# Kernel tuning notes

Hardware: AMD Instinct MI355X
Metric: run time of the kernel (lower is better)

Reference implementation:

```python
import jax, jax.numpy as jnp
import numpy as np

D = 1024; NH = 16; HD = 64; FF = 4096; DEPTH = 4
P = 14; C = 3; GRID = 32; MERGE = 2; NIMG = 4
L = GRID * GRID; S = NIMG * L; ORIG = 24; EPS = 1e-6
SCALE = HD ** -0.5


def setup_inputs() -> dict:
    key = jax.random.key(0)
    ks = jax.random.split(key, 12)
    s = 0.02
    return {
        "pixel_values": jax.random.normal(ks[0], (S, C * P * P), jnp.float32),
        "grid_thw": jnp.tile(jnp.array([[1, GRID, GRID]], jnp.int32), (NIMG, 1)),
        "conv_w": jax.random.normal(ks[1], (D, C * P * P), jnp.float32) * s,
        "conv_b": jnp.zeros((D,), jnp.float32),
        "pos_embed": jax.random.normal(ks[2], (ORIG * ORIG, D), jnp.float32) * s,
        "ln1_g": jnp.ones((DEPTH, D), jnp.float32),
        "ln1_b": jnp.zeros((DEPTH, D), jnp.float32),
        "qkv_w": jax.random.normal(ks[3], (DEPTH, 3 * D, D), jnp.float32) * s,
        "qkv_b": jnp.zeros((DEPTH, 3 * D), jnp.float32),
        "proj_w": jax.random.normal(ks[4], (DEPTH, D, D), jnp.float32) * s,
        "proj_b": jnp.zeros((DEPTH, D), jnp.float32),
        "ln2_g": jnp.ones((DEPTH, D), jnp.float32),
        "ln2_b": jnp.zeros((DEPTH, D), jnp.float32),
        "fc1_w": jax.random.normal(ks[5], (DEPTH, FF, D), jnp.float32) * s,
        "fc1_b": jnp.zeros((DEPTH, FF), jnp.float32),
        "fc2_w": jax.random.normal(ks[6], (DEPTH, D, FF), jnp.float32) * s,
        "fc2_b": jnp.zeros((DEPTH, D), jnp.float32),
    }


def _pos_ids():
    # rot_pos_emb spatial-merge permutation for one t=1 image, tiled over images
    h = jnp.broadcast_to(jnp.arange(GRID)[:, None], (GRID, GRID))
    w = jnp.broadcast_to(jnp.arange(GRID)[None, :], (GRID, GRID))
    def perm(a):
        a = a.reshape(GRID // MERGE, MERGE, GRID // MERGE, MERGE)
        return a.transpose(0, 2, 1, 3).reshape(-1)
    hpos = jnp.tile(perm(h), NIMG)  # [S]
    wpos = jnp.tile(perm(w), NIMG)
    return hpos, wpos


def _bilinear_border(img, nx, ny):
    # img [H, W, D]; nx, ny in [-1, 1]; align_corners=False, padding_mode='border'
    Hh, Ww, _ = img.shape
    x = (nx + 1.0) * 0.5 * Ww - 0.5
    y = (ny + 1.0) * 0.5 * Hh - 0.5
    x0 = jnp.floor(x); y0 = jnp.floor(y)
    wx = (x - x0)[:, None]; wy = (y - y0)[:, None]
    x0i = jnp.clip(x0.astype(jnp.int32), 0, Ww - 1)
    x1i = jnp.clip(x0.astype(jnp.int32) + 1, 0, Ww - 1)
    y0i = jnp.clip(y0.astype(jnp.int32), 0, Hh - 1)
    y1i = jnp.clip(y0.astype(jnp.int32) + 1, 0, Hh - 1)
    v00 = img[y0i, x0i]; v01 = img[y0i, x1i]
    v10 = img[y1i, x0i]; v11 = img[y1i, x1i]
    return (v00 * (1 - wy) * (1 - wx) + v01 * (1 - wy) * wx
            + v10 * wy * (1 - wx) + v11 * wy * wx)


def _ln(x, g, b):
    m = jnp.mean(x, axis=-1, keepdims=True)
    v = jnp.mean(jnp.square(x - m), axis=-1, keepdims=True)
    return (x - m) * jax.lax.rsqrt(v + EPS) * g + b


def _forward(pixel_values, conv_w, conv_b, pos_embed, ln1_g, ln1_b, qkv_w, qkv_b,
             proj_w, proj_b, ln2_g, ln2_b, fc1_w, fc1_b, fc2_w, fc2_b):
    # patch embed: conv with kernel==stride==patch over one patch == linear
    x = pixel_values @ conv_w.T + conv_b  # [S, D]

    # interpolated 2D position embedding (grid_sample bilinear, border pad)
    hpos, wpos = _pos_ids()
    norm_w = (wpos.astype(jnp.float32) + 0.5) / GRID * 2.0 - 1.0
    norm_h = (hpos.astype(jnp.float32) + 0.5) / GRID * 2.0 - 1.0
    pe = _bilinear_border(pos_embed.reshape(ORIG, ORIG, D), norm_w, norm_h)
    x = x + pe

    for i in range(DEPTH):
        # attention (block-diagonal over equal-length images -> batched)
        r = x
        y = _ln(x, ln1_g[i], ln1_b[i])
        qkv = (y @ qkv_w[i].T + qkv_b[i]).reshape(NIMG, L, 3, NH, HD)
        q = qkv[:, :, 0].transpose(0, 2, 1, 3)  # [B, H, L, hd]
        k = qkv[:, :, 1].transpose(0, 2, 1, 3)
        v = qkv[:, :, 2].transpose(0, 2, 1, 3)
        scores = jnp.einsum('bhqd,bhkd->bhqk', q, k) * SCALE
        probs = jax.nn.softmax(scores, axis=-1)
        o = jnp.einsum('bhqk,bhkd->bhqd', probs, v)
        o = o.transpose(0, 2, 1, 3).reshape(S, D)
        x = r + o @ proj_w[i].T + proj_b[i]
        # MLP
        r = x
        y = _ln(x, ln2_g[i], ln2_b[i])
        h = jax.nn.gelu(y @ fc1_w[i].T + fc1_b[i], approximate=False)
        x = r + h @ fc2_w[i].T + fc2_b[i]
    return x


def reference(pixel_values, grid_thw, conv_w, conv_b, pos_embed, ln1_g, ln1_b,
              qkv_w, qkv_b, proj_w, proj_b, ln2_g, ln2_b, fc1_w, fc1_b, fc2_w, fc2_b):
    return _forward(pixel_values, conv_w, conv_b, pos_embed, ln1_g, ln1_b, qkv_w,
                    qkv_b, proj_w, proj_b, ln2_g, ln2_b, fc1_w, fc1_b, fc2_w, fc2_b)
```

## Files before the change

### kernel.cpp

```cpp
#include <hip/hip_runtime.h>
#include <math.h>

typedef __bf16 bf16x8 __attribute__((ext_vector_type(8)));
typedef float f32x4 __attribute__((ext_vector_type(4)));
typedef short s16x4 __attribute__((ext_vector_type(4)));
typedef short s16x8 __attribute__((ext_vector_type(8)));

static __device__ __forceinline__ short f2bs(float f) {
  return __builtin_bit_cast(short, (__bf16)f);
}

#define GLL16(gp, lp) __builtin_amdgcn_global_load_lds( \
    (const __attribute__((address_space(1))) void*)(gp), \
    (__attribute__((address_space(3))) void*)(lp), 16, 0, 0)

__global__ __launch_bounds__(256) void cvt_f32_bf16(const float* __restrict__ s,
                                                    short* __restrict__ d, int n) {
  int stride = gridDim.x * blockDim.x * 4;
  for (int j = (blockIdx.x * blockDim.x + threadIdx.x) * 4; j < n; j += stride) {
    float4 v = *(const float4*)(s + j);
    s16x4 o;
    o[0] = f2bs(v.x); o[1] = f2bs(v.y); o[2] = f2bs(v.z); o[3] = f2bs(v.w);
    *(s16x4*)(d + j) = o;
  }
}

__global__ __launch_bounds__(256) void cvt_pad(const float* __restrict__ s,
                                               short* __restrict__ d) {
  int r = blockIdx.x;
  for (int c = threadIdx.x; c < 608; c += blockDim.x)
    d[(size_t)r * 608 + c] = (c < 588) ? f2bs(s[(size_t)r * 588 + c]) : (short)0;
}

template <int N, int K, int EPI, int CM, int CN>
__global__ __launch_bounds__(256) void gemm_bt(const short* __restrict__ A,
                                               const short* __restrict__ B,
                                               const float* __restrict__ bias,
                                               const float* __restrict__ resid,
                                               void* __restrict__ out) {
  static_assert(K % 32 == 0, "K");
  constexpr int NT = K / 32;
  static_assert(NT >= 3, "pipeline depth");
  constexpr int NX = N / 128, NY = 32;
  constexpr int nwg = NX * NY;
  static_assert(nwg % 8 == 0 && (nwg / 8) % (CM * CN) == 0, "chunk");
  static_assert(NX % CN == 0 && NY % CM == 0, "cells");
  __shared__ short lA[3][128 * 32];
  __shared__ short lB[3][128 * 32];

  const int o = blockIdx.x;
  const int wid = (o & 7) * (nwg / 8) + (o >> 3);
  constexpr int cellsz = CM * CN;
  const int cell = wid / cellsz, within = wid % cellsz;
  constexpr int cellsx = NX / CN;
  const int bm0 = ((cell / cellsx) * CM + within / CN) * 128;
  const int bn0 = ((cell % cellsx) * CN + within % CN) * 128;

  const int t = threadIdx.x, w = t >> 6, lane = t & 63;
  const int wr = w >> 1, wc = w & 1;
  f32x4 acc[4][4] = {};

  const int srow = t >> 2;
  const int scol = ((t & 3) ^ ((srow >> 1) & 3)) * 8;
  const short* aP = A + (size_t)(bm0 + srow) * K + scol;
  const short* bP = B + (size_t)(bn0 + srow) * K + scol;
  const int sdst0 = (w * 16) * 32;
  const int sdst1 = (64 + w * 16) * 32;

  const int lr = lane & 15;
  const int qx = ((lane >> 4) ^ ((lr >> 1) & 3)) * 8;

  auto stage = [&](int buf, int ko) {
    GLL16(aP + ko, &lA[buf][sdst0]);
    GLL16(aP + ko + (size_t)64 * K, &lA[buf][sdst1]);
    GLL16(bP + ko, &lB[buf][sdst0]);
    GLL16(bP + ko + (size_t)64 * K, &lB[buf][sdst1]);
  };

  stage(0, 0);
  stage(1, 32);
  stage(2, 64);

  int buf = 0;
  for (int kt = 0; kt < NT; ++kt) {
    if (kt < NT - 2)       asm volatile("s_waitcnt vmcnt(8)" ::: "memory");
    else if (kt == NT - 2) asm volatile("s_waitcnt vmcnt(4)" ::: "memory");
    else                   asm volatile("s_waitcnt vmcnt(0)" ::: "memory");
    __builtin_amdgcn_s_barrier();
    asm volatile("" ::: "memory");
    __builtin_amdgcn_sched_barrier(0);

    bf16x8 af[4], bg[4];
#pragma unroll
    for (int mi = 0; mi < 4; ++mi)
      af[mi] = *(const bf16x8*)&lA[buf][(wr * 64 + mi * 16 + lr) * 32 + qx];
#pragma unroll
    for (int ni = 0; ni < 4; ++ni)
      bg[ni] = *(const bf16x8*)&lB[buf][(wc * 64 + ni * 16 + lr) * 32 + qx];

    asm volatile("s_waitcnt lgkmcnt(0)" ::: "memory");
    __builtin_amdgcn_sched_barrier(0);
    __builtin_amdgcn_s_barrier();
    asm volatile("" ::: "memory");
    __builtin_amdgcn_sched_barrier(0);

    if (kt + 3 < NT) stage(buf, (kt + 3) * 32);
    __builtin_amdgcn_sched_barrier(0);

#pragma unroll
    for (int mi = 0; mi < 4; ++mi)
#pragma unroll
      for (int ni = 0; ni < 4; ++ni)
        acc[mi][ni] = __builtin_amdgcn_mfma_f32_16x16x32_bf16(af[mi], bg[ni],
                                                              acc[mi][ni], 0, 0, 0);
    buf = (buf == 2) ? 0 : buf + 1;
  }

  const int lg4 = (lane >> 4) * 4;
#pragma unroll
  for (int mi = 0; mi < 4; ++mi) {
#pragma unroll
    for (int ni = 0; ni < 4; ++ni) {
      const int row = bm0 + wr * 64 + mi * 16 + lg4;
      const int col = bn0 + wc * 64 + ni * 16 + lr;
      const float bc = bias[col];
#pragma unroll
      for (int r = 0; r < 4; ++r) {
        float v = acc[mi][ni][r] + bc;
        size_t idx = (size_t)(row + r) * N + col;
        if constexpr (EPI == 1) v = 0.5f * v * (1.0f + erff(v * 0.70710678118f));
        if constexpr (EPI == 0 || EPI == 1) ((short*)out)[idx] = f2bs(v);
        else if constexpr (EPI == 2) ((float*)out)[idx] = v + resid[idx];
        else ((float*)out)[idx] = v;
      }
    }
  }
}

__global__ __launch_bounds__(256) void ln_fwd(const float* __restrict__ x,
                                              const float* __restrict__ g,
                                              const float* __restrict__ b,
                                              short* __restrict__ y) {
  const int row = blockIdx.x, t = threadIdx.x, w = t >> 6, lane = t & 63;
  const float4 v = ((const float4*)(x + (size_t)row * 1024))[t];
  float s = v.x + v.y + v.z + v.w;
  float ss = v.x * v.x + v.y * v.y + v.z * v.z + v.w * v.w;
#pragma unroll
  for (int m = 1; m < 64; m <<= 1) { s += __shfl_xor(s, m); ss += __shfl_xor(ss, m); }
  __shared__ float rs[4], rss[4];
  if (lane == 0) { rs[w] = s; rss[w] = ss; }
  __syncthreads();
  s = rs[0] + rs[1] + rs[2] + rs[3];
  ss = rss[0] + rss[1] + rss[2] + rss[3];
  const float mean = s * (1.f / 1024.f);
  const float var = ss * (1.f / 1024.f) - mean * mean;
  const float rstd = rsqrtf(var + 1e-6f);
  const float4 gv = ((const float4*)g)[t];
  const float4 bv = ((const float4*)b)[t];
  s16x4 o;
  o[0] = f2bs((v.x - mean) * rstd * gv.x + bv.x);
  o[1] = f2bs((v.y - mean) * rstd * gv.y + bv.y);
  o[2] = f2bs((v.z - mean) * rstd * gv.z + bv.z);
  o[3] = f2bs((v.w - mean) * rstd * gv.w + bv.w);
  *(s16x4*)(y + (size_t)row * 1024 + t * 4) = o;
}

__global__ __launch_bounds__(256) void pos_add(float* __restrict__ x,
                                               const float* __restrict__ pe) {
  const int sidx = blockIdx.x;
  const int f = sidx & 1023;
  const int wq = 2 * ((f >> 2) & 15) + (f & 1);
  const int hq = 2 * (f >> 6) + ((f >> 1) & 1);
  const float gx = (wq + 0.5f) * 0.75f - 0.5f;
  const float gy = (hq + 0.5f) * 0.75f - 0.5f;
  const float fx = floorf(gx), fy = floorf(gy);
  const float wx = gx - fx, wy = gy - fy;
  int x0 = (int)fx, y0 = (int)fy;
  const int x0i = x0 < 0 ? 0 : (x0 > 23 ? 23 : x0);
  const int x1i = (x0 + 1) < 0 ? 0 : ((x0 + 1) > 23 ? 23 : x0 + 1);
  const int y0i = y0 < 0 ? 0 : (y0 > 23 ? 23 : y0);
  const int y1i = (y0 + 1) < 0 ? 0 : ((y0 + 1) > 23 ? 23 : y0 + 1);
  const float w00 = (1 - wy) * (1 - wx), w01 = (1 - wy) * wx;
  const float w10 = wy * (1 - wx), w11 = wy * wx;
  const int c = threadIdx.x * 4;
  const float4 p00 = *(const float4*)(pe + (size_t)(y0i * 24 + x0i) * 1024 + c);
  const float4 p01 = *(const float4*)(pe + (size_t)(y0i * 24 + x1i) * 1024 + c);
  const float4 p10 = *(const float4*)(pe + (size_t)(y1i * 24 + x0i) * 1024 + c);
  const float4 p11 = *(const float4*)(pe + (size_t)(y1i * 24 + x1i) * 1024 + c);
  float* xp = x + (size_t)sidx * 1024 + c;
  float4 xv = *(float4*)xp;
  xv.x += w00 * p00.x + w01 * p01.x + w10 * p10.x + w11 * p11.x;
  xv.y += w00 * p00.y + w01 * p01.y + w10 * p10.y + w11 * p11.y;
  xv.z += w00 * p00.z + w01 * p01.z + w10 * p10.z + w11 * p11.z;
  xv.w += w00 * p00.w + w01 * p01.w + w10 * p10.w + w11 * p11.w;
  *(float4*)xp = xv;
}

__global__ __launch_bounds__(256) void attn_fwd(const short* __restrict__ qkv,
                                                short* __restrict__ outp) {
  __shared__ short lK[2][64 * 64];
  __shared__ short Vt[2][64 * 72];
  const int t = threadIdx.x, w = t >> 6, lane = t & 63;
  const int b = blockIdx.y >> 4, h = blockIdx.y & 15;
  const int sbase = b * 1024;
  const int q0 = blockIdx.x * 64 + w * 16;
  const int lr = lane & 15, lg = lane >> 4;

  const short* qrow = qkv + (size_t)(sbase + q0 + lr) * 3072 + h * 64;
  const bf16x8 qf0 = *(const bf16x8*)(qrow + lg * 8);
  const bf16x8 qf1 = *(const bf16x8*)(qrow + 32 + lg * 8);

  const int krofs = t >> 3;
  const int kcol = ((t & 7) ^ (krofs & 7)) * 8;
  const short* ksrc = qkv + (size_t)(sbase + krofs) * 3072 + 1024 + h * 64 + kcol;
  const int vkv = t >> 2, vdp = t & 3;
  const short* vsrc = qkv + (size_t)(sbase + vkv) * 3072 + 2048 + h * 64 + vdp * 16;
  const int vph = vkv ^ (vdp << 4);

  f32x4 o[4] = {};
  float mrun = -1e30f, lsum = 0.f;

  s16x8 v0 = *(const s16x8*)vsrc;
  s16x8 v1 = *(const s16x8*)(vsrc + 8);
  GLL16(ksrc, &lK[0][(w * 8) * 64]);
  GLL16(ksrc + (size_t)32 * 3072, &lK[0][(32 + w * 8) * 64]);
#pragma unroll
  for (int j = 0; j < 8; ++j) Vt[0][(vdp * 16 + j) * 72 + vph] = v0[j];
#pragma unroll
  for (int j = 0; j < 8; ++j) Vt[0][(vdp * 16 + 8 + j) * 72 + vph] = v1[j];
  asm volatile("s_waitcnt vmcnt(0) lgkmcnt(0)" ::: "memory");
  __builtin_amdgcn_s_barrier();

  int buf = 0;
  for (int kb = 0; kb < 16; ++kb) {
    if (kb < 15) {
      const short* vs = vsrc + (size_t)(kb + 1) * 64 * 3072;
      v0 = *(const s16x8*)vs;
      v1 = *(const s16x8*)(vs + 8);
      const short* ks = ksrc + (size_t)(kb + 1) * 64 * 3072;
      GLL16(ks, &lK[buf ^ 1][(w * 8) * 64]);
      GLL16(ks + (size_t)32 * 3072, &lK[buf ^ 1][(32 + w * 8) * 64]);
    }

    f32x4 s[4];
    __builtin_amdgcn_s_setprio(1);
#pragma unroll
    for (int sub = 0; sub < 4; ++sub) {
      const int krow = (sub * 16 + lr) * 64;
      const bf16x8 kf0 = *(const bf16x8*)&lK[buf][krow + (lg ^ (lr & 7)) * 8];
      const bf16x8 kf1 = *(const bf16x8*)&lK[buf][krow + ((lg + 4) ^ (lr & 7)) * 8];
      f32x4 a = {};
      a = __builtin_amdgcn_mfma_f32_16x16x32_bf16(kf0, qf0, a, 0, 0, 0);
      a = __builtin_amdgcn_mfma_f32_16x16x32_bf16(kf1, qf1, a, 0, 0, 0);
      s[sub] = a;
    }
    __builtin_amdgcn_s_setprio(0);

    constexpr float SC = 0.125f * 1.44269504089f;
    float sl[16];
#pragma unroll
    for (int sub = 0; sub < 4; ++sub)
#pragma unroll
      for (int r = 0; r < 4; ++r) sl[sub * 4 + r] = s[sub][r] * SC;
    float tm = sl[0];
#pragma unroll
    for (int i = 1; i < 16; ++i) tm = fmaxf(tm, sl[i]);
    tm = fmaxf(tm, __shfl_xor(tm, 16));
    tm = fmaxf(tm, __shfl_xor(tm, 32));
    if (!__all(tm <= mrun + 12.0f)) {
      const float newm = fmaxf(mrun, tm);
      const float sc = exp2f(mrun - newm);
      lsum *= sc;
#pragma unroll
      for (int f = 0; f < 4; ++f) {
        o[f][0] *= sc; o[f][1] *= sc; o[f][2] *= sc; o[f][3] *= sc;
      }
      mrun = newm;
    }
    s16x4 pb[4];
    float psum = 0.f;
#pragma unroll
    for (int sub = 0; sub < 4; ++sub)
#pragma unroll
      for (int r = 0; r < 4; ++r) {
        const float p = exp2f(sl[sub * 4 + r] - mrun);
        psum += p;
        pb[sub][r] = f2bs(p);
      }
    psum += __shfl_xor(psum, 16);
    psum += __shfl_xor(psum, 32);
    lsum += psum;

    __builtin_amdgcn_s_setprio(1);
#pragma unroll
    for (int f = 0; f < 4; ++f) {
      const int vrow = (f * 16 + lr) * 72;
#pragma unroll
      for (int sub = 0; sub < 4; ++sub) {
        const s16x4 va = *(const s16x4*)&Vt[buf][vrow + ((sub ^ f) << 4) + lg * 4];
        o[f] = __builtin_amdgcn_mfma_f32_16x16x16bf16_1k(va, pb[sub], o[f], 0, 0, 0);
      }
    }
    __builtin_amdgcn_s_setprio(0);

    if (kb < 15) {
#pragma unroll
      for (int j = 0; j < 8; ++j) Vt[buf ^ 1][(vdp * 16 + j) * 72 + vph] = v0[j];
#pragma unroll
      for (int j = 0; j < 8; ++j) Vt[buf ^ 1][(vdp * 16 + 8 + j) * 72 + vph] = v1[j];
      asm volatile("s_waitcnt vmcnt(0) lgkmcnt(0)" ::: "memory");
      __builtin_amdgcn_s_barrier();
      buf ^= 1;
    }
  }

  const float inv = 1.0f / lsum;
  short* orow = outp + (size_t)(sbase + q0 + lr) * 1024 + h * 64;
#pragma unroll
  for (int f = 0; f < 4; ++f) {
    s16x4 ov;
    ov[0] = f2bs(o[f][0] * inv); ov[1] = f2bs(o[f][1] * inv);
    ov[2] = f2bs(o[f][2] * inv); ov[3] = f2bs(o[f][3] * inv);
    *(s16x4*)(orow + f * 16 + lg * 4) = ov;
  }
}

extern "C" void kernel_launch(void* const* d_in, const int* in_sizes, int n_in,
                              void* d_out, int out_size, void* d_ws, size_t ws_size,
                              hipStream_t stream) {
  const float* pixel  = (const float*)d_in[0];
  const float* conv_w = (const float*)d_in[2];
  const float* conv_b = (const float*)d_in[3];
  const float* pos_e  = (const float*)d_in[4];
  const float* ln1_g  = (const float*)d_in[5];
  const float* ln1_b  = (const float*)d_in[6];
  const float* qkv_w  = (const float*)d_in[7];
  const float* qkv_b  = (const float*)d_in[8];
  const float* proj_w = (const float*)d_in[9];
  const float* proj_b = (const float*)d_in[10];
  const float* ln2_g  = (const float*)d_in[11];
  const float* ln2_b  = (const float*)d_in[12];
  const float* fc1_w  = (const float*)d_in[13];
  const float* fc1_b  = (const float*)d_in[14];
  const float* fc2_w  = (const float*)d_in[15];
  const float* fc2_b  = (const float*)d_in[16];

  char* ws = (char*)d_ws;
  short* wQKV  = (short*)(ws + 0);
  short* wPROJ = (short*)(ws + 25165824);
  short* wFC1  = (short*)(ws + 33554432);
  short* wFC2  = (short*)(ws + 67108864);
  float* X     = (float*)(ws + 100663296);
  short* Y     = (short*)(ws + 117440512);
  short* QKVB  = (short*)(ws + 125829120);
  short* ATTNO = (short*)(ws + 150994944);
  short* H     = QKVB;
  short* WPIX  = QKVB;
  short* WCONV = (short*)(ws + 125829120 + 4980736);

  cvt_f32_bf16<<<2048, 256, 0, stream>>>(qkv_w, wQKV, 4 * 3072 * 1024);
  cvt_f32_bf16<<<1024, 256, 0, stream>>>(proj_w, wPROJ, 4 * 1024 * 1024);
  cvt_f32_bf16<<<2048, 256, 0, stream>>>(fc1_w, wFC1, 4 * 4096 * 1024);
  cvt_f32_bf16<<<2048, 256, 0, stream>>>(fc2_w, wFC2, 4 * 1024 * 4096);
  cvt_pad<<<4096, 256, 0, stream>>>(pixel, WPIX);
  cvt_pad<<<1024, 256, 0, stream>>>(conv_w, WCONV);

  gemm_bt<1024, 608, 3, 4, 8><<<256, 256, 0, stream>>>(WPIX, WCONV, conv_b, nullptr, X);
  pos_add<<<4096, 256, 0, stream>>>(X, pos_e);

  for (int i = 0; i < 4; ++i) {
    ln_fwd<<<4096, 256, 0, stream>>>(X, ln1_g + i * 1024, ln1_b + i * 1024, Y);
    gemm_bt<3072, 1024, 0, 8, 12><<<768, 256, 0, stream>>>(
        Y, wQKV + (size_t)i * 3072 * 1024, qkv_b + i * 3072, nullptr, QKVB);
    attn_fwd<<<dim3(16, 64), 256, 0, stream>>>(QKVB, ATTNO);
    gemm_bt<1024, 1024, 2, 4, 8><<<256, 256, 0, stream>>>(
        ATTNO, wPROJ + (size_t)i * 1024 * 1024, proj_b + i * 1024, X, X);
    ln_fwd<<<4096, 256, 0, stream>>>(X, ln2_g + i * 1024, ln2_b + i * 1024, Y);
    gemm_bt<4096, 1024, 1, 16, 8><<<1024, 256, 0, stream>>>(
        Y, wFC1 + (size_t)i * 4096 * 1024, fc1_b + i * 4096, nullptr, H);
    float* dest = (i < 3) ? X : (float*)d_out;
    gemm_bt<1024, 4096, 2, 4, 8><<<256, 256, 0, stream>>>(
        H, wFC2 + (size_t)i * 1024 * 4096, fc2_b + i * 1024, X, dest);
  }
}
```

Baseline: 1.043 ms.

## Add 256x256-tile 512-thread pipelined GEMM for QKV and FC1 projections

Introduces a new GEMM kernel with 256x256 output tiles, 8 waves per block, double-buffered LDS staged through global_load_lds, a phased schedule that interleaves LDS reads, MFMA bursts and prefetches with explicit barriers and waitcnts, plus an XCD-aware block remap. The QKV and FC1 GEMMs switch to it. The aim is more operand reuse per LDS load and better overlap of memory traffic with MFMA. The cost is fewer blocks (192 and 256) and a higher register and LDS footprint, which can limit occupancy on the machine.

```diff
diff --git a/kernel.cpp b/kernel.cpp
--- a/kernel.cpp
+++ b/kernel.cpp
@@ -132,6 +132,141 @@
         if constexpr (EPI == 0 || EPI == 1) ((short*)out)[idx] = f2bs(v);
         else if constexpr (EPI == 2) ((float*)out)[idx] = v + resid[idx];
         else ((float*)out)[idx] = v;
+      }
+    }
+  }
+}
+
+template <int N, int K, int EPI, int CM, int CN>
+__global__ __launch_bounds__(512, 2) void gemm256(const short* __restrict__ A,
+                                                  const short* __restrict__ B,
+                                                  const float* __restrict__ bias,
+                                                  void* __restrict__ out) {
+  static_assert(K % 64 == 0, "K");
+  constexpr int NKT = K / 64;
+  static_assert(NKT >= 3 && (NKT % 2) == 0, "ktiles");
+  constexpr int NXT = N / 256, MYT = 16;
+  constexpr int nwg = NXT * MYT;
+  static_assert(nwg % 8 == 0 && (nwg / 8) % (CM * CN) == 0, "chunk");
+  static_assert(NXT % CN == 0 && MYT % CM == 0, "cells");
+
+  __shared__ short sA[2][2][8192];
+  __shared__ short sB[2][2][8192];
+
+  const int o = blockIdx.x;
+  const int wid = (o & 7) * (nwg / 8) + (o >> 3);
+  constexpr int cellsz = CM * CN;
+  const int cell = wid / cellsz, within = wid % cellsz;
+  constexpr int cellsx = NXT / CN;
+  const int bm0 = ((cell / cellsx) * CM + within / CN) * 256;
+  const int bn0 = ((cell % cellsx) * CN + within % CN) * 256;
+
+  const int tid = threadIdx.x, wv = tid >> 6, lane = tid & 63;
+  const int wrow = wv >> 2, wcol = wv & 3;
+  const int lr = lane & 15, lg = lane >> 4;
+
+  const int sr0 = tid >> 2;
+  const int sc0 = ((tid & 3) ^ (sr0 & 3)) * 8;
+  const short* aS0 = A + (size_t)(bm0 + sr0) * K + sc0;
+  const short* bS0 = B + (size_t)(bn0 + sr0) * K + sc0;
+  const int ld0 = wv * 512, ld1 = 4096 + wv * 512;
+
+  auto stageA = [&](int d, int h, int kt) {
+    const int off = kt * 64 + h * 32;
+    GLL16(aS0 + off, &sA[d][h][ld0]);
+    GLL16(aS0 + off + (size_t)128 * K, &sA[d][h][ld1]);
+  };
+  auto stageB = [&](int d, int h, int kt) {
+    const int off = kt * 64 + h * 32;
+    GLL16(bS0 + off, &sB[d][h][ld0]);
+    GLL16(bS0 + off + (size_t)128 * K, &sB[d][h][ld1]);
+  };
+
+  const int chR = (lg ^ (lr & 3)) * 8;
+  const int rA0 = wrow * 128 + lr;
+  const int rB0 = wcol * 64 + lr;
+
+  f32x4 acc[8][4] = {};
+
+  stageA(0, 0, 0); stageB(0, 0, 0);
+  stageA(0, 1, 0); stageB(0, 1, 0);
+  stageA(1, 0, 1); stageB(1, 0, 1);
+  asm volatile("s_waitcnt vmcnt(8)" ::: "memory");
+  __builtin_amdgcn_sched_barrier(0);
+  __builtin_amdgcn_s_barrier();
+
+  bf16x8 af[4], bf[4];
+
+#define LDA(mh, ks, d)                                                        \
+  _Pragma("unroll")                                                           \
+  for (int f = 0; f < 4; ++f)                                                 \
+    af[f] = *(const bf16x8*)&sA[d][ks][(rA0 + (mh)*64 + f * 16) * 32 + chR];
+#define LDB(ks, d)                                                            \
+  _Pragma("unroll")                                                           \
+  for (int n = 0; n < 4; ++n)                                                 \
+    bf[n] = *(const bf16x8*)&sB[d][ks][(rB0 + n * 16) * 32 + chR];
+#define MFMA16(mh)                                                            \
+  __builtin_amdgcn_s_setprio(1);                                              \
+  _Pragma("unroll")                                                           \
+  for (int f = 0; f < 4; ++f)                                                 \
+    _Pragma("unroll")                                                         \
+    for (int n = 0; n < 4; ++n)                                               \
+      acc[(mh)*4 + f][n] = __builtin_amdgcn_mfma_f32_16x16x32_bf16(           \
+          af[f], bf[n], acc[(mh)*4 + f][n], 0, 0, 0);                         \
+  __builtin_amdgcn_s_setprio(0);
+#define PH_BAR1                                                               \
+  __builtin_amdgcn_s_barrier();                                               \
+  asm volatile("s_waitcnt lgkmcnt(0)" ::: "memory");                          \
+  __builtin_amdgcn_sched_barrier(0);
+#define PH_END                                                                \
+  __builtin_amdgcn_s_barrier();
+#define PH_END_V                                                              \
+  asm volatile("s_waitcnt vmcnt(8)" ::: "memory");                            \
+  __builtin_amdgcn_sched_barrier(0);                                          \
+  __builtin_amdgcn_s_barrier();
+
+  for (int t = 0; t < NKT; ++t) {
+    const int d = t & 1;
+    int t1 = t + 1; if (t1 >= NKT) t1 -= NKT;
+    int t2 = t + 2; if (t2 >= NKT) t2 -= NKT;
+    const int d1 = t1 & 1, d2 = t2 & 1;
+
+    LDA(0, 0, d); LDB(0, d);
+    stageA(d1, 1, t1);
+    PH_BAR1; MFMA16(0); PH_END;
+    LDA(1, 0, d);
+    stageB(d1, 1, t1);
+    PH_BAR1; MFMA16(1); PH_END_V;
+    LDA(0, 1, d); LDB(1, d);
+    stageA(d2, 0, t2);
+    PH_BAR1; MFMA16(0); PH_END;
+    LDA(1, 1, d);
+    stageB(d2, 0, t2);
+    PH_BAR1; MFMA16(1); PH_END_V;
+  }
+#undef LDA
+#undef LDB
+#undef MFMA16
+#undef PH_BAR1
+#undef PH_END
+#undef PH_END_V
+
+  const int lg4 = lg * 4;
+#pragma unroll
+  for (int mh = 0; mh < 2; ++mh) {
+#pragma unroll
+    for (int f = 0; f < 4; ++f) {
+#pragma unroll
+      for (int n = 0; n < 4; ++n) {
+        const int row = bm0 + wrow * 128 + mh * 64 + f * 16 + lg4;
+        const int col = bn0 + wcol * 64 + n * 16 + lr;
+        const float bc = bias[col];
+#pragma unroll
+        for (int r = 0; r < 4; ++r) {
+          float v = acc[mh * 4 + f][n][r] + bc;
+          if constexpr (EPI == 1) v = 0.5f * v * (1.0f + erff(v * 0.70710678118f));
+          ((short*)out)[(size_t)(row + r) * N + col] = f2bs(v);
+        }
       }
     }
   }
@@ -370,14 +505,14 @@
 
   for (int i = 0; i < 4; ++i) {
     ln_fwd<<<4096, 256, 0, stream>>>(X, ln1_g + i * 1024, ln1_b + i * 1024, Y);
-    gemm_bt<3072, 1024, 0, 8, 12><<<768, 256, 0, stream>>>(
-        Y, wQKV + (size_t)i * 3072 * 1024, qkv_b + i * 3072, nullptr, QKVB);
+    gemm256<3072, 1024, 0, 8, 3><<<192, 512, 0, stream>>>(
+        Y, wQKV + (size_t)i * 3072 * 1024, qkv_b + i * 3072, QKVB);
     attn_fwd<<<dim3(16, 64), 256, 0, stream>>>(QKVB, ATTNO);
     gemm_bt<1024, 1024, 2, 4, 8><<<256, 256, 0, stream>>>(
         ATTNO, wPROJ + (size_t)i * 1024 * 1024, proj_b + i * 1024, X, X);
     ln_fwd<<<4096, 256, 0, stream>>>(X, ln2_g + i * 1024, ln2_b + i * 1024, Y);
-    gemm_bt<4096, 1024, 1, 16, 8><<<1024, 256, 0, stream>>>(
-        Y, wFC1 + (size_t)i * 4096 * 1024, fc1_b + i * 4096, nullptr, H);
+    gemm256<4096, 1024, 1, 8, 4><<<256, 512, 0, stream>>>(
+        Y, wFC1 + (size_t)i * 4096 * 1024, fc1_b + i * 4096, H);
     float* dest = (i < 3) ? X : (float*)d_out;
     gemm_bt<1024, 4096, 2, 4, 8><<<256, 256, 0, stream>>>(
         H, wFC2 + (size_t)i * 1024 * 4096, fc2_b + i * 1024, X, dest);
```

New measurement: 1.063 ms. Within noise of the previous version (+1.9%).

## Add double-buffered 128x128 GEMM with split-K FC2 and tanh GELU

Applied to the files above, without the earlier changes.

Adds a new 128x128-tile bf16 MFMA GEMM that uses two LDS buffers with async global-to-LDS loads, an XCD-aware tile swizzle, and occupancy 2. It is used for the QKV and FC1 GEMMs, and for FC2 it runs as a split-K kernel writing fp32 partials that a separate reduce kernel sums together with bias and residual. The FC1 epilogue switches from the exact erf GELU to a tanh-form approximation computed with exp. The aim is better latency hiding and more workgroups for the thin FC2 GEMM. In exchange it adds traffic for the partial sums and slightly changes the GELU numerics.

```diff
diff --git a/kernel.cpp b/kernel.cpp
--- a/kernel.cpp
+++ b/kernel.cpp
@@ -135,6 +135,139 @@
       }
     }
   }
+}
+
+template <int N, int KC, int LDK, int EPI, int CM, int CN, int KSPLIT>
+__global__ __launch_bounds__(256, 2) void gemm128(const short* __restrict__ A,
+                                                  const short* __restrict__ B,
+                                                  const float* __restrict__ bias,
+                                                  void* __restrict__ out) {
+  static_assert(KC % 64 == 0, "K");
+  constexpr int NKT = KC / 64;
+  static_assert(NKT >= 4 && (NKT % 2) == 0, "ktiles");
+  constexpr int NX = N / 128, NY = 32;
+  constexpr int nwg = NX * NY * KSPLIT;
+  constexpr int cellsz = CM * CN;
+  static_assert(nwg % 8 == 0 && (nwg / 8) % cellsz == 0, "chunk");
+  static_assert((NX * NY) % cellsz == 0, "cellspace");
+  static_assert(NX % CN == 0 && NY % CM == 0, "cells");
+
+  __shared__ short sA[2][128 * 64];
+  __shared__ short sB[2][128 * 64];
+
+  const int o = blockIdx.x;
+  const int wid = (o & 7) * (nwg / 8) + (o >> 3);
+  const int kc = wid / (NX * NY);
+  const int rem = wid % (NX * NY);
+  const int cell = rem / cellsz, within = rem % cellsz;
+  constexpr int cellsx = NX / CN;
+  const int bm0 = ((cell / cellsx) * CM + within / CN) * 128;
+  const int bn0 = ((cell % cellsx) * CN + within % CN) * 128;
+
+  const int t = threadIdx.x, w = t >> 6, lane = t & 63;
+  const int wr = w >> 1, wc = w & 1;
+  const int lr = lane & 15, lg = lane >> 4;
+
+  const int srow = t >> 3;
+  const int sch = (t & 7) ^ (srow & 7);
+  const short* aS = A + (size_t)(bm0 + srow) * LDK + kc * KC + sch * 8;
+  const short* bS = B + (size_t)(bn0 + srow) * LDK + kc * KC + sch * 8;
+  const int ldst = w * 512;
+
+  auto stage = [&](int d, int kt) {
+    const size_t ko = (size_t)kt * 64;
+#pragma unroll
+    for (int q = 0; q < 4; ++q)
+      GLL16(aS + (size_t)q * 32 * LDK + ko, &sA[d][q * 2048 + ldst]);
+#pragma unroll
+    for (int q = 0; q < 4; ++q)
+      GLL16(bS + (size_t)q * 32 * LDK + ko, &sB[d][q * 2048 + ldst]);
+  };
+
+  f32x4 acc[4][4] = {};
+
+  stage(0, 0);
+  stage(1, 1);
+
+#define TILE(tt, dd)                                                          \
+  {                                                                           \
+    if ((tt) + 1 < NKT) asm volatile("s_waitcnt vmcnt(8)" ::: "memory");      \
+    else                asm volatile("s_waitcnt vmcnt(0)" ::: "memory");      \
+    __builtin_amdgcn_s_barrier();                                             \
+    bf16x8 af[2][4], bf[2][4];                                                \
+    _Pragma("unroll")                                                         \
+    for (int ks = 0; ks < 2; ++ks) {                                          \
+      _Pragma("unroll")                                                       \
+      for (int mi = 0; mi < 4; ++mi)                                          \
+        af[ks][mi] = *(const bf16x8*)&sA[dd][(wr * 64 + mi * 16 + lr) * 64 +  \
+                                             (((ks << 2) + lg) ^ (lr & 7)) * 8]; \
+      _Pragma("unroll")                                                       \
+      for (int ni = 0; ni < 4; ++ni)                                          \
+        bf[ks][ni] = *(const bf16x8*)&sB[dd][(wc * 64 + ni * 16 + lr) * 64 +  \
+                                             (((ks << 2) + lg) ^ (lr & 7)) * 8]; \
+    }                                                                         \
+    __builtin_amdgcn_s_setprio(1);                                            \
+    _Pragma("unroll")                                                         \
+    for (int ks = 0; ks < 2; ++ks)                                            \
+      _Pragma("unroll")                                                       \
+      for (int mi = 0; mi < 4; ++mi)                                          \
+        _Pragma("unroll")                                                     \
+        for (int ni = 0; ni < 4; ++ni)                                        \
+          acc[mi][ni] = __builtin_amdgcn_mfma_f32_16x16x32_bf16(              \
+              af[ks][mi], bf[ks][ni], acc[mi][ni], 0, 0, 0);                  \
+    __builtin_amdgcn_s_setprio(0);                                            \
+    __builtin_amdgcn_s_barrier();                                             \
+    if ((tt) + 2 < NKT) stage(dd, (tt) + 2);                                  \
+  }
+
+  for (int kt = 0; kt < NKT; kt += 2) {
+    TILE(kt, 0);
+    TILE(kt + 1, 1);
+  }
+#undef TILE
+
+  const int lg4 = lg * 4;
+#pragma unroll
+  for (int mi = 0; mi < 4; ++mi) {
+#pragma unroll
+    for (int ni = 0; ni < 4; ++ni) {
+      const int row = bm0 + wr * 64 + mi * 16 + lg4;
+      const int col = bn0 + wc * 64 + ni * 16 + lr;
+      float bc = 0.f;
+      if constexpr (EPI != 5) bc = bias[col];
+#pragma unroll
+      for (int r = 0; r < 4; ++r) {
+        float v = acc[mi][ni][r] + bc;
+        if constexpr (EPI == 1) {
+          const float u = v * (0.7978845608f + 0.0356774081f * v * v);
+          v = v / (1.0f + __expf(-2.0f * u));
+        }
+        if constexpr (EPI == 5)
+          ((float*)out)[((size_t)kc << 22) + (size_t)(row + r) * N + col] = v;
+        else
+          ((short*)out)[(size_t)(row + r) * N + col] = f2bs(v);
+      }
+    }
+  }
+}
+
+__global__ __launch_bounds__(256) void fc2_reduce(const float* __restrict__ part,
+                                                  const float* __restrict__ bias,
+                                                  const float* __restrict__ resid,
+                                                  float* __restrict__ dest) {
+  const size_t i4 = ((size_t)blockIdx.x * 256 + threadIdx.x) * 4;
+  const float4 a0 = *(const float4*)(part + i4);
+  const float4 a1 = *(const float4*)(part + (1ull << 22) + i4);
+  const float4 a2 = *(const float4*)(part + (2ull << 22) + i4);
+  const float4 a3 = *(const float4*)(part + (3ull << 22) + i4);
+  const float4 rv = *(const float4*)(resid + i4);
+  const float4 bv = *(const float4*)(bias + (i4 & 1023));
+  float4 o;
+  o.x = a0.x + a1.x + a2.x + a3.x + rv.x + bv.x;
+  o.y = a0.y + a1.y + a2.y + a3.y + rv.y + bv.y;
+  o.z = a0.z + a1.z + a2.z + a3.z + rv.z + bv.z;
+  o.w = a0.w + a1.w + a2.w + a3.w + rv.w + bv.w;
+  *(float4*)(dest + i4) = o;
 }
 
 __global__ __launch_bounds__(256) void ln_fwd(const float* __restrict__ x,
@@ -357,6 +490,8 @@
   short* H     = QKVB;
   short* WPIX  = QKVB;
   short* WCONV = (short*)(ws + 125829120 + 4980736);
+  float* PART  = (float*)(ws + 159383552);
+  const bool wsbig = ws_size >= (size_t)159383552 + 67108864;
 
   cvt_f32_bf16<<<2048, 256, 0, stream>>>(qkv_w, wQKV, 4 * 3072 * 1024);
   cvt_f32_bf16<<<1024, 256, 0, stream>>>(proj_w, wPROJ, 4 * 1024 * 1024);
@@ -370,16 +505,22 @@
 
   for (int i = 0; i < 4; ++i) {
     ln_fwd<<<4096, 256, 0, stream>>>(X, ln1_g + i * 1024, ln1_b + i * 1024, Y);
-    gemm_bt<3072, 1024, 0, 8, 12><<<768, 256, 0, stream>>>(
-        Y, wQKV + (size_t)i * 3072 * 1024, qkv_b + i * 3072, nullptr, QKVB);
+    gemm128<3072, 1024, 1024, 0, 8, 4, 1><<<768, 256, 0, stream>>>(
+        Y, wQKV + (size_t)i * 3072 * 1024, qkv_b + i * 3072, QKVB);
     attn_fwd<<<dim3(16, 64), 256, 0, stream>>>(QKVB, ATTNO);
     gemm_bt<1024, 1024, 2, 4, 8><<<256, 256, 0, stream>>>(
         ATTNO, wPROJ + (size_t)i * 1024 * 1024, proj_b + i * 1024, X, X);
     ln_fwd<<<4096, 256, 0, stream>>>(X, ln2_g + i * 1024, ln2_b + i * 1024, Y);
-    gemm_bt<4096, 1024, 1, 16, 8><<<1024, 256, 0, stream>>>(
-        Y, wFC1 + (size_t)i * 4096 * 1024, fc1_b + i * 4096, nullptr, H);
+    gemm128<4096, 1024, 1024, 1, 8, 4, 1><<<1024, 256, 0, stream>>>(
+        Y, wFC1 + (size_t)i * 4096 * 1024, fc1_b + i * 4096, H);
     float* dest = (i < 3) ? X : (float*)d_out;
-    gemm_bt<1024, 4096, 2, 4, 8><<<256, 256, 0, stream>>>(
-        H, wFC2 + (size_t)i * 1024 * 4096, fc2_b + i * 1024, X, dest);
-  }
-}
+    if (wsbig) {
+      gemm128<1024, 1024, 4096, 5, 8, 4, 4><<<1024, 256, 0, stream>>>(
+          H, wFC2 + (size_t)i * 1024 * 4096, nullptr, PART);
+      fc2_reduce<<<4096, 256, 0, stream>>>(PART, fc2_b + i * 1024, X, dest);
+    } else {
+      gemm_bt<1024, 4096, 2, 4, 8><<<256, 256, 0, stream>>>(
+          H, wFC2 + (size_t)i * 1024 * 4096, fc2_b + i * 1024, X, dest);
+    }
+  }
+}
```

Result: faster. 1.013 ms (-2.9%).
